# Optimization experiments

Measured on AMD Instinct MI355X. Metric: run time of the kernel, lower is better.

Reference implementation:

```python
import jax, jax.numpy as jnp
import numpy as np

EPS = 1e-07
NEG = -1e9


def setup_inputs() -> dict:
    key = jax.random.key(0)
    k1, k2, k3, k4 = jax.random.split(key, 4)
    N, M, D = 8192, 8192, 128
    xi = jax.random.normal(k1, (N, D), dtype=jnp.float32)
    xj = jax.random.normal(k2, (M, D), dtype=jnp.float32)
    adj = jax.random.randint(k3, (N, M), 0, 2, dtype=jnp.int32)
    beta = jax.random.uniform(k4, (1,), dtype=jnp.float32)
    return {"xi": xi, "xj": xj, "adj": adj, "beta": beta}


def reference(xi, xj, adj, beta):
    # cosine similarity scores, scaled by learned beta
    xi_norm = jnp.linalg.norm(xi, ord=2, axis=1, keepdims=True)      # [N,1]
    xj_norm = jnp.linalg.norm(xj, ord=2, axis=1, keepdims=True).T    # [1,M]
    cos = beta * (xi @ xj.T) / (xi_norm * xj_norm + EPS)             # [N,M]
    # additive adjacency mask: non-edges pushed to -1e9
    mask = (1.0 - adj.astype(cos.dtype)) * NEG
    P = jax.nn.softmax(cos + mask, axis=1)                           # [N,M]
    return P @ xj                                                    # [N,D]
```

## Files before the change

### kernel.cpp

```cpp
#include <hip/hip_runtime.h>
#include <hip/hip_bf16.h>

typedef float f32x4 __attribute__((ext_vector_type(4)));
typedef short s16x8 __attribute__((ext_vector_type(8)));
typedef unsigned long long ull;

#define NROWS 8192
#define MCOLS 8192
#define DIM   128
#define JSPLIT 8
#define JCHUNK 1024
#define KVB    64
#define ITERS  16

typedef __attribute__((address_space(3))) unsigned int lds_u32;
typedef __attribute__((address_space(1))) unsigned int g_u32;

__device__ __forceinline__ void gl_lds16(const void* g, void* l) {
    __builtin_amdgcn_global_load_lds((const g_u32*)g, (lds_u32*)l, 16, 0, 0);
}

__global__ __launch_bounds__(256) void prep_all(const float* __restrict__ xi,
                                                const float* __restrict__ xj,
                                                const float* __restrict__ beta,
                                                const int* __restrict__ adj,
                                                __hip_bfloat16* __restrict__ Qbf,
                                                __hip_bfloat16* __restrict__ Kbf,
                                                __hip_bfloat16* __restrict__ Vt,
                                                ull* __restrict__ bm) {
    __shared__ float tile[64][65];
    const int tid  = threadIdx.x;
    const int w    = tid >> 6;
    const int lane = tid & 63;

    {
        float b = beta[0];
#pragma unroll
        for (int sub = 0; sub < 2; ++sub) {
            int gr = blockIdx.x * 8 + w * 2 + sub;
            const float* src;
            __hip_bfloat16* dst;
            int row;
            if (gr < NROWS) { row = gr;          src = xi; dst = Qbf; }
            else            { row = gr - NROWS;  src = xj; dst = Kbf; }
            const float* xr = src + (size_t)row * DIM;
            float x0 = xr[lane], x1 = xr[lane + 64];
            float ss = x0 * x0 + x1 * x1;
#pragma unroll
            for (int off = 32; off >= 1; off >>= 1) ss += __shfl_xor(ss, off);
            float s = 1.0f / sqrtf(ss);
            if (gr < NROWS) s *= b;
            __hip_bfloat16* o = dst + (size_t)row * DIM;
            o[lane]      = __float2bfloat16(x0 * s);
            o[lane + 64] = __float2bfloat16(x1 * s);
        }
    }

    if (blockIdx.x < 256) {
        int j0 = (blockIdx.x & 127) * 64;
        int d0 = (blockIdx.x >> 7) * 64;
#pragma unroll
        for (int c = 0; c < 16; ++c) {
            int idx = tid + 256 * c;
            int jr = idx >> 6, dc = idx & 63;
            tile[jr][dc] = xj[(size_t)(j0 + jr) * DIM + d0 + dc];
        }
        __syncthreads();
#pragma unroll
        for (int c = 0; c < 16; ++c) {
            int idx = tid + 256 * c;
            int dr = idx >> 6, jc = idx & 63;
            Vt[(size_t)(d0 + dr) * MCOLS + j0 + jc] = __float2bfloat16(tile[jc][dr]);
        }
        __syncthreads();
    }

    const int gw = (int)((blockIdx.x * 256 + tid) >> 6);
#pragma unroll 2
    for (int s = 0; s < 32; ++s) {
        int win = gw + s * 8192;
        const int* base = adj + (size_t)win * 256;
        int a0 = base[lane], a1 = base[64 + lane], a2 = base[128 + lane], a3 = base[192 + lane];
        ull b0 = __ballot(a0 != 0);
        ull b1 = __ballot(a1 != 0);
        ull b2 = __ballot(a2 != 0);
        ull b3 = __ballot(a3 != 0);
        if (lane < 4) {
            ull v = (lane == 0) ? b0 : ((lane == 1) ? b1 : ((lane == 2) ? b2 : b3));
            bm[(size_t)win * 4 + lane] = v;
        }
    }
}

__global__ __launch_bounds__(256, 2) void flash10(const __hip_bfloat16* __restrict__ Qbf,
                                                  const __hip_bfloat16* __restrict__ Kbf,
                                                  const __hip_bfloat16* __restrict__ Vt,
                                                  const ull* __restrict__ bm,
                                                  float* __restrict__ Opart,
                                                  float* __restrict__ Lpart) {
    __shared__ char smem[81920];

    const int tid  = threadIdx.x;
    const int w    = tid >> 6;
    const int lane = tid & 63;
    const int g    = lane >> 4;
    const int ln   = lane & 15;
    const int bid  = blockIdx.x;
    const int jc   = bid & (JSPLIT - 1);
    const int rt   = bid >> 3;
    const int wra  = rt * 128 + w * 32;
    const int jbase = jc * JCHUNK;
    const int lx   = ln & 7;

    s16x8 qf[2][4];
#pragma unroll
    for (int ti = 0; ti < 2; ++ti)
#pragma unroll
        for (int kt = 0; kt < 4; ++kt)
            qf[ti][kt] = *(const s16x8*)(Qbf + (size_t)(wra + ti * 16 + ln) * DIM + kt * 32 + g * 8);

    f32x4 zero = {0.f, 0.f, 0.f, 0.f};
    f32x4 acc[2][8];
#pragma unroll
    for (int ti = 0; ti < 2; ++ti)
#pragma unroll
        for (int dt = 0; dt < 8; ++dt) acc[ti][dt] = zero;
    float lr[2][4] = {{0.f, 0.f, 0.f, 0.f}, {0.f, 0.f, 0.f, 0.f}};

    char* pw = smem + 65536 + w * 4096;

    auto STAGE = [&](int jt, int b) {
        char* kb = smem + b * 16384;
        char* vb = smem + 32768 + b * 16384;
#pragma unroll
        for (int p = 0; p < 4; ++p) {
            int S = p * 256 + tid;
            int row = S >> 4, u = S & 15;
            gl_lds16((const char*)Kbf + (((size_t)(jt + row)) << 8) + ((u ^ (row & 7)) << 4),
                     kb + p * 4096 + w * 1024);
        }
#pragma unroll
        for (int p = 0; p < 4; ++p) {
            int S = p * 256 + tid;
            int row = S >> 3, u = S & 7;
            gl_lds16((const char*)Vt + (((size_t)row) << 14) + (((size_t)jt) << 1) + ((u ^ (row & 7)) << 4),
                     vb + p * 4096 + w * 1024);
        }
    };

    STAGE(jbase, 0);
    __syncthreads();
    int cur = 0;

    for (int it = 0; it < ITERS; ++it) {
        const int jt = jbase + it * KVB;

        ull mw[2][4];
#pragma unroll
        for (int ti = 0; ti < 2; ++ti)
#pragma unroll
            for (int r = 0; r < 4; ++r)
                mw[ti][r] = bm[(size_t)(wra + ti * 16 + g * 4 + r) * 128 + (jt >> 6)];
        __builtin_amdgcn_sched_barrier(0);

        STAGE(jbase + ((it + 1) & (ITERS - 1)) * KVB, cur ^ 1);

        const char* kb = smem + cur * 16384;
        const char* vb = smem + 32768 + cur * 16384;

        f32x4 s4[2][4];
#pragma unroll
        for (int ti = 0; ti < 2; ++ti)
#pragma unroll
            for (int ct = 0; ct < 4; ++ct) s4[ti][ct] = zero;
#pragma unroll
        for (int ct = 0; ct < 4; ++ct)
#pragma unroll
            for (int kt = 0; kt < 4; ++kt) {
                s16x8 kf = *(const s16x8*)(kb + (ct * 16 + ln) * 256 + (((kt * 4 + g) ^ lx) << 4));
                s4[0][ct] = __builtin_amdgcn_mfma_f32_16x16x32_bf16(qf[0][kt], kf, s4[0][ct], 0, 0, 0);
                s4[1][ct] = __builtin_amdgcn_mfma_f32_16x16x32_bf16(qf[1][kt], kf, s4[1][ct], 0, 0, 0);
            }

#pragma unroll
        for (int ti = 0; ti < 2; ++ti)
#pragma unroll
            for (int r = 0; r < 4; ++r) {
                const int row = g * 4 + r;
                const int rs = row & 7;
#pragma unroll
                for (int ct = 0; ct < 4; ++ct) {
                    float p = ((mw[ti][r] >> (ct * 16 + ln)) & 1) ? __expf(s4[ti][ct][r]) : 0.f;
                    lr[ti][r] += p;
                    *(__hip_bfloat16*)(pw + ti * 2048 + row * 128 +
                                       (((ct * 2 + (ln >> 3)) ^ rs) << 4) + (ln & 7) * 2)
                        = __float2bfloat16(p);
                }
            }

#pragma unroll
        for (int kt2 = 0; kt2 < 2; ++kt2) {
            const int uo = ((kt2 * 4 + g) ^ lx) << 4;
            s16x8 pf0 = *(const s16x8*)(pw + ln * 128 + uo);
            s16x8 pf1 = *(const s16x8*)(pw + 2048 + ln * 128 + uo);
#pragma unroll
            for (int dt = 0; dt < 8; ++dt) {
                s16x8 vf = *(const s16x8*)(vb + (dt * 16 + ln) * 128 + uo);
                acc[0][dt] = __builtin_amdgcn_mfma_f32_16x16x32_bf16(pf0, vf, acc[0][dt], 0, 0, 0);
                acc[1][dt] = __builtin_amdgcn_mfma_f32_16x16x32_bf16(pf1, vf, acc[1][dt], 0, 0, 0);
            }
        }

        __syncthreads();
        cur ^= 1;
    }

#pragma unroll
    for (int ti = 0; ti < 2; ++ti)
#pragma unroll
        for (int r = 0; r < 4; ++r) {
            lr[ti][r] += __shfl_xor(lr[ti][r], 1);
            lr[ti][r] += __shfl_xor(lr[ti][r], 2);
            lr[ti][r] += __shfl_xor(lr[ti][r], 4);
            lr[ti][r] += __shfl_xor(lr[ti][r], 8);
        }

#pragma unroll
    for (int ti = 0; ti < 2; ++ti) {
        float* ob = Opart + ((size_t)jc * NROWS + wra + ti * 16 + g * 4) * DIM;
#pragma unroll
        for (int r = 0; r < 4; ++r)
#pragma unroll
            for (int dt = 0; dt < 8; ++dt)
                ob[(size_t)r * DIM + dt * 16 + ln] = acc[ti][dt][r];
        if (ln == 0) {
#pragma unroll
            for (int r = 0; r < 4; ++r)
                Lpart[(size_t)jc * NROWS + wra + ti * 16 + g * 4 + r] = lr[ti][r];
        }
    }
}

__global__ __launch_bounds__(256) void merge10(const float* __restrict__ Opart,
                                               const float* __restrict__ Lpart,
                                               float* __restrict__ out) {
    int gid = blockIdx.x * 256 + threadIdx.x;
    int row = gid >> 5;
    int dq  = (gid & 31) * 4;
    float4 sum = {0.f, 0.f, 0.f, 0.f};
    float L = 0.f;
#pragma unroll
    for (int jc = 0; jc < JSPLIT; ++jc) {
        float4 v = *(const float4*)(Opart + ((size_t)jc * NROWS + row) * DIM + dq);
        sum.x += v.x; sum.y += v.y; sum.z += v.z; sum.w += v.w;
        L += Lpart[(size_t)jc * NROWS + row];
    }
    float inv = 1.0f / fmaxf(L, 1e-37f);
    float4 ov = {sum.x * inv, sum.y * inv, sum.z * inv, sum.w * inv};
    *(float4*)(out + (size_t)row * DIM + dq) = ov;
}

extern "C" void kernel_launch(void* const* d_in, const int* in_sizes, int n_in,
                              void* d_out, int out_size, void* d_ws, size_t ws_size,
                              hipStream_t stream) {
    const float* xi   = (const float*)d_in[0];
    const float* xj   = (const float*)d_in[1];
    const int*   adj  = (const int*)d_in[2];
    const float* beta = (const float*)d_in[3];
    float* out = (float*)d_out;

    char* ws = (char*)d_ws;
    __hip_bfloat16* Qbf = (__hip_bfloat16*)ws;
    __hip_bfloat16* Kbf = (__hip_bfloat16*)(ws + (size_t)NROWS * DIM * 2);
    __hip_bfloat16* Vt  = (__hip_bfloat16*)(ws + 2 * (size_t)NROWS * DIM * 2);
    ull*            bm  = (ull*)(ws + 3 * (size_t)NROWS * DIM * 2);
    float*          Op  = (float*)(ws + 3 * (size_t)NROWS * DIM * 2 + (size_t)NROWS * (MCOLS / 8));
    float*          Lp  = (float*)((char*)Op + (size_t)JSPLIT * NROWS * DIM * 4);

    hipLaunchKernelGGL(prep_all, dim3(2048), dim3(256), 0, stream, xi, xj, beta, adj, Qbf, Kbf, Vt, bm);
    hipLaunchKernelGGL(flash10, dim3(64 * JSPLIT), dim3(256), 0, stream, Qbf, Kbf, Vt, bm, Op, Lp);
    hipLaunchKernelGGL(merge10, dim3(1024), dim3(256), 0, stream, Op, Lp, out);
}
```

Before: 118.5 us.

## Fuse adjacency bitmask construction into flash kernel with prefetched adj loads

Removes the separate pass in the prep kernel that compressed the int32 adjacency matrix into a bitmask. The flash kernel now reads adj directly with nontemporal loads, prefetching the next tile's 32 rows into registers while the current tile computes, then ballots them into mask words. It also staggers each block's starting KV tile by row-tile index to spread memory traffic. This saves one write and one read of the bitmask but adds 32 registers per lane and 256 MB of adj reads inside the compute kernel, which may hurt occupancy and overlap.

```diff
diff --git a/kernel.cpp b/kernel.cpp
--- a/kernel.cpp
+++ b/kernel.cpp
@@ -20,14 +20,12 @@
     __builtin_amdgcn_global_load_lds((const g_u32*)g, (lds_u32*)l, 16, 0, 0);
 }
 
-__global__ __launch_bounds__(256) void prep_all(const float* __restrict__ xi,
-                                                const float* __restrict__ xj,
-                                                const float* __restrict__ beta,
-                                                const int* __restrict__ adj,
-                                                __hip_bfloat16* __restrict__ Qbf,
-                                                __hip_bfloat16* __restrict__ Kbf,
-                                                __hip_bfloat16* __restrict__ Vt,
-                                                ull* __restrict__ bm) {
+__global__ __launch_bounds__(256) void prep11(const float* __restrict__ xi,
+                                              const float* __restrict__ xj,
+                                              const float* __restrict__ beta,
+                                              __hip_bfloat16* __restrict__ Qbf,
+                                              __hip_bfloat16* __restrict__ Kbf,
+                                              __hip_bfloat16* __restrict__ Vt) {
     __shared__ float tile[64][65];
     const int tid  = threadIdx.x;
     const int w    = tid >> 6;
@@ -72,30 +70,13 @@
             int dr = idx >> 6, jc = idx & 63;
             Vt[(size_t)(d0 + dr) * MCOLS + j0 + jc] = __float2bfloat16(tile[jc][dr]);
         }
-        __syncthreads();
-    }
-
-    const int gw = (int)((blockIdx.x * 256 + tid) >> 6);
-#pragma unroll 2
-    for (int s = 0; s < 32; ++s) {
-        int win = gw + s * 8192;
-        const int* base = adj + (size_t)win * 256;
-        int a0 = base[lane], a1 = base[64 + lane], a2 = base[128 + lane], a3 = base[192 + lane];
-        ull b0 = __ballot(a0 != 0);
-        ull b1 = __ballot(a1 != 0);
-        ull b2 = __ballot(a2 != 0);
-        ull b3 = __ballot(a3 != 0);
-        if (lane < 4) {
-            ull v = (lane == 0) ? b0 : ((lane == 1) ? b1 : ((lane == 2) ? b2 : b3));
-            bm[(size_t)win * 4 + lane] = v;
-        }
-    }
-}
-
-__global__ __launch_bounds__(256, 2) void flash10(const __hip_bfloat16* __restrict__ Qbf,
+    }
+}
+
+__global__ __launch_bounds__(256, 2) void flash11(const __hip_bfloat16* __restrict__ Qbf,
                                                   const __hip_bfloat16* __restrict__ Kbf,
                                                   const __hip_bfloat16* __restrict__ Vt,
-                                                  const ull* __restrict__ bm,
+                                                  const int* __restrict__ adj,
                                                   float* __restrict__ Opart,
                                                   float* __restrict__ Lpart) {
     __shared__ char smem[81920];
@@ -111,6 +92,7 @@
     const int wra  = rt * 128 + w * 32;
     const int jbase = jc * JCHUNK;
     const int lx   = ln & 7;
+    const int itoff = rt & 15;
 
     s16x8 qf[2][4];
 #pragma unroll
@@ -128,6 +110,7 @@
     float lr[2][4] = {{0.f, 0.f, 0.f, 0.f}, {0.f, 0.f, 0.f, 0.f}};
 
     char* pw = smem + 65536 + w * 4096;
+    const int* arow = adj + (size_t)wra * MCOLS + lane;
 
     auto STAGE = [&](int jt, int b) {
         char* kb = smem + b * 16384;
@@ -148,22 +131,38 @@
         }
     };
 
-    STAGE(jbase, 0);
+    int av[32];
+    {
+        const int jt0 = jbase + itoff * KVB;
+        STAGE(jt0, 0);
+#pragma unroll
+        for (int u = 0; u < 32; ++u)
+            av[u] = __builtin_nontemporal_load(arow + (size_t)u * MCOLS + jt0);
+    }
     __syncthreads();
+    ull mw[2][4];
+#pragma unroll
+    for (int ti = 0; ti < 2; ++ti)
+#pragma unroll
+        for (int r = 0; r < 4; ++r) mw[ti][r] = 0;
+#pragma unroll
+    for (int u = 0; u < 32; ++u) {
+        ull b = __ballot(av[u] != 0);
+        mw[u >> 4][u & 3] = (((u & 15) >> 2) == g) ? b : mw[u >> 4][u & 3];
+    }
+
     int cur = 0;
-
     for (int it = 0; it < ITERS; ++it) {
-        const int jt = jbase + it * KVB;
-
-        ull mw[2][4];
-#pragma unroll
-        for (int ti = 0; ti < 2; ++ti)
-#pragma unroll
-            for (int r = 0; r < 4; ++r)
-                mw[ti][r] = bm[(size_t)(wra + ti * 16 + g * 4 + r) * 128 + (jt >> 6)];
+        const int jt  = jbase + ((it + itoff) & (ITERS - 1)) * KVB;
+        const int jtn = jbase + ((it + 1 + itoff) & (ITERS - 1)) * KVB;
+
+#pragma unroll
+        for (int u = 0; u < 32; ++u)
+            av[u] = __builtin_nontemporal_load(arow + (size_t)u * MCOLS + jtn);
         __builtin_amdgcn_sched_barrier(0);
 
-        STAGE(jbase + ((it + 1) & (ITERS - 1)) * KVB, cur ^ 1);
+        STAGE(jtn, cur ^ 1);
+        __builtin_amdgcn_sched_barrier(0);
 
         const char* kb = smem + cur * 16384;
         const char* vb = smem + 32768 + cur * 16384;
@@ -211,6 +210,16 @@
             }
         }
 
+#pragma unroll
+        for (int ti = 0; ti < 2; ++ti)
+#pragma unroll
+            for (int r = 0; r < 4; ++r) mw[ti][r] = 0;
+#pragma unroll
+        for (int u = 0; u < 32; ++u) {
+            ull b = __ballot(av[u] != 0);
+            mw[u >> 4][u & 3] = (((u & 15) >> 2) == g) ? b : mw[u >> 4][u & 3];
+        }
+
         __syncthreads();
         cur ^= 1;
     }
@@ -241,7 +250,7 @@
     }
 }
 
-__global__ __launch_bounds__(256) void merge10(const float* __restrict__ Opart,
+__global__ __launch_bounds__(256) void merge11(const float* __restrict__ Opart,
                                                const float* __restrict__ Lpart,
                                                float* __restrict__ out) {
     int gid = blockIdx.x * 256 + threadIdx.x;
@@ -273,11 +282,10 @@
     __hip_bfloat16* Qbf = (__hip_bfloat16*)ws;
     __hip_bfloat16* Kbf = (__hip_bfloat16*)(ws + (size_t)NROWS * DIM * 2);
     __hip_bfloat16* Vt  = (__hip_bfloat16*)(ws + 2 * (size_t)NROWS * DIM * 2);
-    ull*            bm  = (ull*)(ws + 3 * (size_t)NROWS * DIM * 2);
-    float*          Op  = (float*)(ws + 3 * (size_t)NROWS * DIM * 2 + (size_t)NROWS * (MCOLS / 8));
+    float*          Op  = (float*)(ws + 3 * (size_t)NROWS * DIM * 2);
     float*          Lp  = (float*)((char*)Op + (size_t)JSPLIT * NROWS * DIM * 4);
 
-    hipLaunchKernelGGL(prep_all, dim3(2048), dim3(256), 0, stream, xi, xj, beta, adj, Qbf, Kbf, Vt, bm);
-    hipLaunchKernelGGL(flash10, dim3(64 * JSPLIT), dim3(256), 0, stream, Qbf, Kbf, Vt, bm, Op, Lp);
-    hipLaunchKernelGGL(merge10, dim3(1024), dim3(256), 0, stream, Op, Lp, out);
-}
+    hipLaunchKernelGGL(prep11, dim3(2048), dim3(256), 0, stream, xi, xj, beta, Qbf, Kbf, Vt);
+    hipLaunchKernelGGL(flash11, dim3(64 * JSPLIT), dim3(256), 0, stream, Qbf, Kbf, Vt, adj, Op, Lp);
+    hipLaunchKernelGGL(merge11, dim3(1024), dim3(256), 0, stream, Op, Lp, out);
+}
```

After: 136.3 us. +14.9%, slower.

## Split key dimension 16 ways with 32-wide KV tiles and smaller LDS footprint

Applied to the files above, without the earlier changes.

Doubles the number of key-column splits so the attention kernel launches 1024 blocks instead of 512, each covering 512 columns in 32-column tiles. LDS use is halved to 40 KB and the occupancy hint in the launch bounds is removed, so more blocks can be resident per CU. The P and V shared-memory layouts and their XOR swizzle are reworked for the narrower tiles. In exchange, the merge kernel reads twice as many partial outputs, and each tile does less MFMA work per barrier and mask-word load.

```diff
diff --git a/kernel.cpp b/kernel.cpp
--- a/kernel.cpp
+++ b/kernel.cpp
@@ -8,9 +8,9 @@
 #define NROWS 8192
 #define MCOLS 8192
 #define DIM   128
-#define JSPLIT 8
-#define JCHUNK 1024
-#define KVB    64
+#define JSPLIT 16
+#define JCHUNK 512
+#define KVB    32
 #define ITERS  16
 
 typedef __attribute__((address_space(3))) unsigned int lds_u32;
@@ -92,13 +92,13 @@
     }
 }
 
-__global__ __launch_bounds__(256, 2) void flash10(const __hip_bfloat16* __restrict__ Qbf,
-                                                  const __hip_bfloat16* __restrict__ Kbf,
-                                                  const __hip_bfloat16* __restrict__ Vt,
-                                                  const ull* __restrict__ bm,
-                                                  float* __restrict__ Opart,
-                                                  float* __restrict__ Lpart) {
-    __shared__ char smem[81920];
+__global__ __launch_bounds__(256) void flash16(const __hip_bfloat16* __restrict__ Qbf,
+                                               const __hip_bfloat16* __restrict__ Kbf,
+                                               const __hip_bfloat16* __restrict__ Vt,
+                                               const ull* __restrict__ bm,
+                                               float* __restrict__ Opart,
+                                               float* __restrict__ Lpart) {
+    __shared__ char smem[40960];
 
     const int tid  = threadIdx.x;
     const int w    = tid >> 6;
@@ -107,10 +107,11 @@
     const int ln   = lane & 15;
     const int bid  = blockIdx.x;
     const int jc   = bid & (JSPLIT - 1);
-    const int rt   = bid >> 3;
+    const int rt   = bid >> 4;
     const int wra  = rt * 128 + w * 32;
     const int jbase = jc * JCHUNK;
     const int lx   = ln & 7;
+    const int swv  = (ln & 3) ^ ((ln >> 2) & 3);
 
     s16x8 qf[2][4];
 #pragma unroll
@@ -127,23 +128,24 @@
         for (int dt = 0; dt < 8; ++dt) acc[ti][dt] = zero;
     float lr[2][4] = {{0.f, 0.f, 0.f, 0.f}, {0.f, 0.f, 0.f, 0.f}};
 
-    char* pw = smem + 65536 + w * 4096;
+    char* pw = smem + 32768 + w * 2048;
 
     auto STAGE = [&](int jt, int b) {
-        char* kb = smem + b * 16384;
-        char* vb = smem + 32768 + b * 16384;
-#pragma unroll
-        for (int p = 0; p < 4; ++p) {
+        char* kb = smem + b * 8192;
+        char* vb = smem + 16384 + b * 8192;
+#pragma unroll
+        for (int p = 0; p < 2; ++p) {
             int S = p * 256 + tid;
             int row = S >> 4, u = S & 15;
             gl_lds16((const char*)Kbf + (((size_t)(jt + row)) << 8) + ((u ^ (row & 7)) << 4),
                      kb + p * 4096 + w * 1024);
         }
 #pragma unroll
-        for (int p = 0; p < 4; ++p) {
+        for (int p = 0; p < 2; ++p) {
             int S = p * 256 + tid;
-            int row = S >> 3, u = S & 7;
-            gl_lds16((const char*)Vt + (((size_t)row) << 14) + (((size_t)jt) << 1) + ((u ^ (row & 7)) << 4),
+            int row = S >> 2, u = S & 3;
+            int sw = (row & 3) ^ ((row >> 2) & 3);
+            gl_lds16((const char*)Vt + (((size_t)row) << 14) + (((size_t)jt) << 1) + ((u ^ sw) << 4),
                      vb + p * 4096 + w * 1024);
         }
     };
@@ -165,16 +167,16 @@
 
         STAGE(jbase + ((it + 1) & (ITERS - 1)) * KVB, cur ^ 1);
 
-        const char* kb = smem + cur * 16384;
-        const char* vb = smem + 32768 + cur * 16384;
-
-        f32x4 s4[2][4];
+        const char* kb = smem + cur * 8192;
+        const char* vb = smem + 16384 + cur * 8192;
+
+        f32x4 s4[2][2];
 #pragma unroll
         for (int ti = 0; ti < 2; ++ti)
 #pragma unroll
-            for (int ct = 0; ct < 4; ++ct) s4[ti][ct] = zero;
-#pragma unroll
-        for (int ct = 0; ct < 4; ++ct)
+            for (int ct = 0; ct < 2; ++ct) s4[ti][ct] = zero;
+#pragma unroll
+        for (int ct = 0; ct < 2; ++ct)
 #pragma unroll
             for (int kt = 0; kt < 4; ++kt) {
                 s16x8 kf = *(const s16x8*)(kb + (ct * 16 + ln) * 256 + (((kt * 4 + g) ^ lx) << 4));
@@ -182,32 +184,30 @@
                 s4[1][ct] = __builtin_amdgcn_mfma_f32_16x16x32_bf16(qf[1][kt], kf, s4[1][ct], 0, 0, 0);
             }
 
+        const int bbase = jt & 32;
 #pragma unroll
         for (int ti = 0; ti < 2; ++ti)
 #pragma unroll
             for (int r = 0; r < 4; ++r) {
                 const int row = g * 4 + r;
-                const int rs = row & 7;
-#pragma unroll
-                for (int ct = 0; ct < 4; ++ct) {
-                    float p = ((mw[ti][r] >> (ct * 16 + ln)) & 1) ? __expf(s4[ti][ct][r]) : 0.f;
+                const int rs = r ^ g;
+#pragma unroll
+                for (int ct = 0; ct < 2; ++ct) {
+                    float p = ((mw[ti][r] >> (bbase + ct * 16 + ln)) & 1) ? __expf(s4[ti][ct][r]) : 0.f;
                     lr[ti][r] += p;
-                    *(__hip_bfloat16*)(pw + ti * 2048 + row * 128 +
+                    *(__hip_bfloat16*)(pw + ti * 1024 + row * 64 +
                                        (((ct * 2 + (ln >> 3)) ^ rs) << 4) + (ln & 7) * 2)
                         = __float2bfloat16(p);
                 }
             }
 
 #pragma unroll
-        for (int kt2 = 0; kt2 < 2; ++kt2) {
-            const int uo = ((kt2 * 4 + g) ^ lx) << 4;
-            s16x8 pf0 = *(const s16x8*)(pw + ln * 128 + uo);
-            s16x8 pf1 = *(const s16x8*)(pw + 2048 + ln * 128 + uo);
+        for (int ti = 0; ti < 2; ++ti) {
+            s16x8 pf = *(const s16x8*)(pw + ti * 1024 + ln * 64 + ((g ^ swv) << 4));
 #pragma unroll
             for (int dt = 0; dt < 8; ++dt) {
-                s16x8 vf = *(const s16x8*)(vb + (dt * 16 + ln) * 128 + uo);
-                acc[0][dt] = __builtin_amdgcn_mfma_f32_16x16x32_bf16(pf0, vf, acc[0][dt], 0, 0, 0);
-                acc[1][dt] = __builtin_amdgcn_mfma_f32_16x16x32_bf16(pf1, vf, acc[1][dt], 0, 0, 0);
+                s16x8 vf = *(const s16x8*)(vb + (dt * 16 + ln) * 64 + ((g ^ swv) << 4));
+                acc[ti][dt] = __builtin_amdgcn_mfma_f32_16x16x32_bf16(pf, vf, acc[ti][dt], 0, 0, 0);
             }
         }
 
@@ -241,7 +241,7 @@
     }
 }
 
-__global__ __launch_bounds__(256) void merge10(const float* __restrict__ Opart,
+__global__ __launch_bounds__(256) void merge16(const float* __restrict__ Opart,
                                                const float* __restrict__ Lpart,
                                                float* __restrict__ out) {
     int gid = blockIdx.x * 256 + threadIdx.x;
@@ -271,13 +271,13 @@
 
     char* ws = (char*)d_ws;
     __hip_bfloat16* Qbf = (__hip_bfloat16*)ws;
-    __hip_bfloat16* Kbf = (__hip_bfloat16*)(ws + (size_t)NROWS * DIM * 2);
-    __hip_bfloat16* Vt  = (__hip_bfloat16*)(ws + 2 * (size_t)NROWS * DIM * 2);
-    ull*            bm  = (ull*)(ws + 3 * (size_t)NROWS * DIM * 2);
-    float*          Op  = (float*)(ws + 3 * (size_t)NROWS * DIM * 2 + (size_t)NROWS * (MCOLS / 8));
-    float*          Lp  = (float*)((char*)Op + (size_t)JSPLIT * NROWS * DIM * 4);
+    __hip_bfloat16* Kbf = (__hip_bfloat16*)(ws + (2u << 20));
+    __hip_bfloat16* Vt  = (__hip_bfloat16*)(ws + (4u << 20));
+    ull*            bm  = (ull*)(ws + (6u << 20));
+    float*          Op  = (float*)(ws + (14u << 20));
+    float*          Lp  = (float*)(ws + (78u << 20));
 
     hipLaunchKernelGGL(prep_all, dim3(2048), dim3(256), 0, stream, xi, xj, beta, adj, Qbf, Kbf, Vt, bm);
-    hipLaunchKernelGGL(flash10, dim3(64 * JSPLIT), dim3(256), 0, stream, Qbf, Kbf, Vt, bm, Op, Lp);
-    hipLaunchKernelGGL(merge10, dim3(1024), dim3(256), 0, stream, Op, Lp, out);
-}
+    hipLaunchKernelGGL(flash16, dim3(64 * JSPLIT), dim3(256), 0, stream, Qbf, Kbf, Vt, bm, Op, Lp);
+    hipLaunchKernelGGL(merge16, dim3(1024), dim3(256), 0, stream, Op, Lp, out);
+}
```

Result: slower. 135.2 us (+14.1%).
